# Performance work log

Hardware: AMD Instinct MI355X
Metric: run time of the kernel (lower is better)

Reference implementation:

```python
import jax, jax.numpy as jnp
import numpy as np


def setup_inputs() -> dict:
    key = jax.random.key(0)
    ks = jax.random.split(key, 4)
    B, C, D, H, W = 2, 128, 16, 16, 16
    scale = 1.0 / np.sqrt(C)
    x = jax.random.normal(ks[0], (B, C, D, H, W), dtype=jnp.float32)
    Wq = jax.random.normal(ks[1], (C, C), dtype=jnp.float32) * scale
    Wk = jax.random.normal(ks[2], (C, C), dtype=jnp.float32) * scale
    Wv = jax.random.normal(ks[3], (C, C), dtype=jnp.float32) * scale
    bq = jnp.zeros((C,), jnp.float32)
    bk = jnp.zeros((C,), jnp.float32)
    bv = jnp.zeros((C,), jnp.float32)
    gamma = jnp.asarray(0.3, jnp.float32)
    return {"x": x, "Wq": Wq, "bq": bq, "Wk": Wk, "bk": bk, "Wv": Wv, "bv": bv, "gamma": gamma}


def reference(x, Wq, bq, Wk, bk, Wv, bv, gamma):
    B, C, D, H, W = x.shape
    N = D * H * W
    xf = x.reshape(B, C, N)  # flatten spatial dims
    # 1x1x1 Conv3d == per-voxel channel mixing
    q = jnp.einsum('oc,bcn->bon', Wq, xf) + bq[:, None]
    k = jnp.einsum('oc,bcn->bon', Wk, xf) + bk[:, None]
    v = jnp.einsum('oc,bcn->bon', Wv, xf) + bv[:, None]
    # attn[b,n,m] = sum_c q[b,c,n] * k[b,c,m], custom 1.3 scale, softmax over m
    attn = jax.nn.softmax(jnp.einsum('bcn,bcm->bnm', q, k) * 1.3, axis=2)
    # out = v @ attn^T : out[b,c,n] = sum_m v[b,c,m] * attn[b,n,m]
    out = jnp.einsum('bcm,bnm->bcn', v, attn)
    return x + gamma * out.reshape(B, C, D, H, W)
```

## Files before the change

### kernel.cpp

```cpp
#include <hip/hip_runtime.h>
#include <hip/hip_bf16.h>

typedef __bf16 bf16x8 __attribute__((ext_vector_type(8)));
typedef __bf16 bf16x4 __attribute__((ext_vector_type(4)));
typedef float  floatx4 __attribute__((ext_vector_type(4)));


#define QSCALE 1.8755035f

__global__ __launch_bounds__(128) void proj_kernel(
    const float* __restrict__ x,
    const float* __restrict__ Wq, const float* __restrict__ bq,
    const float* __restrict__ Wk, const float* __restrict__ bk,
    const float* __restrict__ Wv, const float* __restrict__ bv,
    __bf16* __restrict__ qT, __bf16* __restrict__ kT, __bf16* __restrict__ vT2)
{
    constexpr int C = 128, N = 4096;
    const int b = blockIdx.z, which = blockIdx.y, n0 = blockIdx.x * 32;
    const int tid = threadIdx.x;
    const int wv = tid >> 6, lane = tid & 63, l15 = lane & 15, quad = lane >> 4;
    const float* W    = (which == 0) ? Wq : (which == 1) ? Wk : Wv;
    const float* bias = (which == 0) ? bq : (which == 1) ? bk : bv;

    __shared__ __bf16 xhi[32][136];
    __shared__ __bf16 xlo[32][136];
    __shared__ __bf16 v_lds[128][40];

    #pragma unroll
    for (int rep = 0; rep < 8; ++rep) {
        const int j = tid + rep * 128;
        const int c = j >> 3, nl4 = (j & 7) * 4;
        const float4 xv = *(const float4*)(x + (size_t)(b * C + c) * N + n0 + nl4);
        #pragma unroll
        for (int r = 0; r < 4; ++r) {
            const float v = (&xv.x)[r];
            const __bf16 h = (__bf16)v;
            xhi[nl4 + r][c] = h;
            xlo[nl4 + r][c] = (__bf16)(v - (float)h);
        }
    }
    __syncthreads();

    bf16x8 xbh[4], xbl[4];
    #pragma unroll
    for (int kk = 0; kk < 4; ++kk) {
        xbh[kk] = *(bf16x8*)(&xhi[wv * 16 + l15][kk * 32 + quad * 8]);
        xbl[kk] = *(bf16x8*)(&xlo[wv * 16 + l15][kk * 32 + quad * 8]);
    }

    floatx4 acc[8];
    const floatx4 fz = {0.f, 0.f, 0.f, 0.f};
    #pragma unroll
    for (int t = 0; t < 8; ++t) acc[t] = fz;

    #pragma unroll
    for (int kk = 0; kk < 4; ++kk)
        #pragma unroll
        for (int ct = 0; ct < 8; ++ct) {
            const float* wp = W + (size_t)(ct * 16 + l15) * C + kk * 32 + quad * 8;
            const float4 w0 = *(const float4*)wp;
            const float4 w1 = *(const float4*)(wp + 4);
            bf16x8 ahi, alo;
            #pragma unroll
            for (int r = 0; r < 4; ++r) {
                const float v0 = (&w0.x)[r]; const __bf16 h0 = (__bf16)v0;
                ahi[r] = h0; alo[r] = (__bf16)(v0 - (float)h0);
                const float v1 = (&w1.x)[r]; const __bf16 h1 = (__bf16)v1;
                ahi[4 + r] = h1; alo[4 + r] = (__bf16)(v1 - (float)h1);
            }
            acc[ct] = __builtin_amdgcn_mfma_f32_16x16x32_bf16(ahi, xbh[kk], acc[ct], 0, 0, 0);
            acc[ct] = __builtin_amdgcn_mfma_f32_16x16x32_bf16(alo, xbh[kk], acc[ct], 0, 0, 0);
            acc[ct] = __builtin_amdgcn_mfma_f32_16x16x32_bf16(ahi, xbl[kk], acc[ct], 0, 0, 0);
        }

    const int n = n0 + wv * 16 + l15;
    if (which < 2) {
        __bf16* dst = (which == 0) ? qT : kT;
        #pragma unroll
        for (int ct = 0; ct < 8; ++ct) {
            const float4 b4 = *(const float4*)(bias + ct * 16 + quad * 4);
            bf16x4 o;
            #pragma unroll
            for (int r = 0; r < 4; ++r) o[r] = (__bf16)(acc[ct][r] + (&b4.x)[r]);
            *(bf16x4*)(dst + (size_t)(b * N + n) * C + ct * 16 + quad * 4) = o;
        }
    } else {
        #pragma unroll
        for (int ct = 0; ct < 8; ++ct) {
            const float4 b4 = *(const float4*)(bias + ct * 16 + quad * 4);
            #pragma unroll
            for (int r = 0; r < 4; ++r)
                v_lds[ct * 16 + quad * 4 + r][wv * 16 + l15] = (__bf16)(acc[ct][r] + (&b4.x)[r]);
        }
        __syncthreads();
        #pragma unroll
        for (int rep = 0; rep < 4; ++rep) {
            const int j = tid + rep * 128;
            const int c = j >> 2, m8 = (j & 3) * 8;
            *(bf16x8*)(vT2 + (size_t)(b * C + c) * N + n0 + m8) = *(bf16x8*)(&v_lds[c][m8]);
        }
    }
}

template <int NSPLIT, bool PARTIAL>
__global__ __launch_bounds__(256, 2) void flash_kernel(
    const __bf16* __restrict__ qT, const __bf16* __restrict__ kT,
    const __bf16* __restrict__ vT2, const float* __restrict__ x,
    const float* __restrict__ gamma_p, __bf16* __restrict__ Opart,
    float* __restrict__ ml, float* __restrict__ out)
{
    constexpr int C = 128, N = 4096, Bn = 2;
    const int bid = blockIdx.x;
    const int r7 = bid & 7;
    const int b = r7 >> 2;
    const int rest = (bid >> 3) * 4 + (r7 & 3);
    const int nt = rest & 63, split = rest >> 6;
    const int n0 = nt * 64;
    const int tid = threadIdx.x;
    const int wv = tid >> 6, lane = tid & 63, l15 = lane & 15, quad = lane >> 4;

    __shared__ __bf16 k_s[64][136];
    __shared__ __bf16 v_s[128][72];
    __shared__ __bf16 p_s[4][16][72];

    const int n = n0 + wv * 16 + l15;
    bf16x8 qb[4];
    #pragma unroll
    for (int kk = 0; kk < 4; ++kk)
        qb[kk] = *(const bf16x8*)(qT + (size_t)(b * N + n) * C + kk * 32 + quad * 8);

    float m_i = -3.0e38f, l_i = 0.f;
    floatx4 Oacc[8];
    const floatx4 fz = {0.f, 0.f, 0.f, 0.f};
    #pragma unroll
    for (int t = 0; t < 8; ++t) Oacc[t] = fz;

    const __bf16* kB = kT  + (size_t)b * N * C;
    const __bf16* vB = vT2 + (size_t)b * C * N;
    constexpr int ITERS = (N / NSPLIT) / 64;
    const int mbeg = split * (N / NSPLIT);

    bf16x8 kpre[4], vpre[4];
    #pragma unroll
    for (int rep = 0; rep < 4; ++rep) {
        const int kj = tid + rep * 256;
        kpre[rep] = *(const bf16x8*)(kB + (size_t)(mbeg + (kj >> 4)) * C + (kj & 15) * 8);
        const int vj = tid + rep * 256;
        vpre[rep] = *(const bf16x8*)(vB + (size_t)(vj >> 3) * N + mbeg + (vj & 7) * 8);
    }

    for (int it = 0; it < ITERS; ++it) {
        __syncthreads();
        #pragma unroll
        for (int rep = 0; rep < 4; ++rep) {
            const int kj = tid + rep * 256;
            *(bf16x8*)(&k_s[kj >> 4][(kj & 15) * 8]) = kpre[rep];
            const int vj = tid + rep * 256;
            *(bf16x8*)(&v_s[vj >> 3][(vj & 7) * 8]) = vpre[rep];
        }
        __syncthreads();

        if (it + 1 < ITERS) {
            const int m1 = mbeg + (it + 1) * 64;
            #pragma unroll
            for (int rep = 0; rep < 4; ++rep) {
                const int kj = tid + rep * 256;
                kpre[rep] = *(const bf16x8*)(kB + (size_t)(m1 + (kj >> 4)) * C + (kj & 15) * 8);
                const int vj = tid + rep * 256;
                vpre[rep] = *(const bf16x8*)(vB + (size_t)(vj >> 3) * N + m1 + (vj & 7) * 8);
            }
        }

        floatx4 S[4];
        #pragma unroll
        for (int ct = 0; ct < 4; ++ct) S[ct] = fz;
        #pragma unroll
        for (int kk = 0; kk < 4; ++kk)
            #pragma unroll
            for (int ct = 0; ct < 4; ++ct) {
                const bf16x8 a = *(bf16x8*)(&k_s[ct * 16 + l15][kk * 32 + quad * 8]);
                S[ct] = __builtin_amdgcn_mfma_f32_16x16x32_bf16(a, qb[kk], S[ct], 0, 0, 0);
            }

        float rmax = -3.0e38f;
        #pragma unroll
        for (int ct = 0; ct < 4; ++ct)
            #pragma unroll
            for (int r = 0; r < 4; ++r) {
                const float v = S[ct][r] * QSCALE;
                S[ct][r] = v;
                rmax = fmaxf(rmax, v);
            }
        rmax = fmaxf(rmax, __shfl_xor(rmax, 16, 64));
        rmax = fmaxf(rmax, __shfl_xor(rmax, 32, 64));

        const float mn = fmaxf(m_i, rmax);
        const float alpha = exp2f(m_i - mn);
        m_i = mn;

        float rsum = 0.f;
        #pragma unroll
        for (int ct = 0; ct < 4; ++ct)
            #pragma unroll
            for (int r = 0; r < 4; ++r) {
                const float p = exp2f(S[ct][r] - m_i);
                S[ct][r] = p;
                rsum += p;
            }
        rsum += __shfl_xor(rsum, 16, 64);
        rsum += __shfl_xor(rsum, 32, 64);
        l_i = l_i * alpha + rsum;

        #pragma unroll
        for (int t = 0; t < 8; ++t)
            #pragma unroll
            for (int r = 0; r < 4; ++r) Oacc[t][r] *= alpha;

        #pragma unroll
        for (int ct = 0; ct < 4; ++ct) {
            bf16x4 pk;
            #pragma unroll
            for (int r = 0; r < 4; ++r) pk[r] = (__bf16)S[ct][r];
            *(bf16x4*)(&p_s[wv][l15][ct * 16 + quad * 4]) = pk;
        }

        #pragma unroll
        for (int kk = 0; kk < 2; ++kk) {
            const bf16x8 pb = *(bf16x8*)(&p_s[wv][l15][kk * 32 + quad * 8]);
            #pragma unroll
            for (int ct = 0; ct < 8; ++ct) {
                const bf16x8 a = *(bf16x8*)(&v_s[ct * 16 + l15][kk * 32 + quad * 8]);
                Oacc[ct] = __builtin_amdgcn_mfma_f32_16x16x32_bf16(a, pb, Oacc[ct], 0, 0, 0);
            }
        }
    }

    if (PARTIAL) {
        __bf16* Op = Opart + (((size_t)split * Bn + b) * N + n) * C;
        #pragma unroll
        for (int ct = 0; ct < 8; ++ct) {
            bf16x4 o;
            #pragma unroll
            for (int r = 0; r < 4; ++r) o[r] = (__bf16)Oacc[ct][r];
            *(bf16x4*)(Op + ct * 16 + quad * 4) = o;
        }
        if (quad == 0) {
            float* mlp = ml + (((size_t)split * Bn + b) * N + n) * 2;
            mlp[0] = m_i; mlp[1] = l_i;
        }
    } else {
        const float sc = 1.f / l_i;
        const float gamma = gamma_p[0];
        #pragma unroll
        for (int ct = 0; ct < 8; ++ct)
            #pragma unroll
            for (int r = 0; r < 4; ++r) {
                const int c = ct * 16 + quad * 4 + r;
                const size_t idx = ((size_t)b * C + c) * N + n;
                out[idx] = x[idx] + gamma * Oacc[ct][r] * sc;
            }
    }
}

__global__ __launch_bounds__(256) void combine_kernel(
    const __bf16* __restrict__ Opart, const float* __restrict__ ml,
    const float* __restrict__ x, const float* __restrict__ gamma_p,
    float* __restrict__ out)
{
    constexpr int C = 128, N = 4096, Bn = 2, S = 4;
    const int b = blockIdx.y, n0 = blockIdx.x * 32;
    const int tid = threadIdx.x;
    __shared__ float cf[S][32];
    __shared__ float ot[32][132];

    if (tid < 32) {
        const int n = n0 + tid;
        float ms[S], ls[S];
        #pragma unroll
        for (int s = 0; s < S; ++s) {
            const float* mlp = ml + (((size_t)s * Bn + b) * N + n) * 2;
            ms[s] = mlp[0]; ls[s] = mlp[1];
        }
        float M = -3.0e38f;
        #pragma unroll
        for (int s = 0; s < S; ++s) M = fmaxf(M, ms[s]);
        float L = 0.f, e[S];
        #pragma unroll
        for (int s = 0; s < S; ++s) { e[s] = exp2f(ms[s] - M); L += e[s] * ls[s]; }
        const float inv = 1.f / L;
        #pragma unroll
        for (int s = 0; s < S; ++s) cf[s][tid] = e[s] * inv;
    }
    __syncthreads();

    #pragma unroll
    for (int rep = 0; rep < 2; ++rep) {
        const int j = tid + rep * 256;
        const int nl = j >> 4, c8 = (j & 15) * 8;
        float acc[8] = {0, 0, 0, 0, 0, 0, 0, 0};
        #pragma unroll
        for (int s = 0; s < S; ++s) {
            const float c0 = cf[s][nl];
            const bf16x8 ov = *(const bf16x8*)(Opart + (((size_t)s * Bn + b) * N + n0 + nl) * C + c8);
            #pragma unroll
            for (int t = 0; t < 8; ++t) acc[t] += c0 * (float)ov[t];
        }
        *(float4*)(&ot[nl][c8])     = *(float4*)(&acc[0]);
        *(float4*)(&ot[nl][c8 + 4]) = *(float4*)(&acc[4]);
    }
    __syncthreads();

    const int nl = tid & 31, cbase = tid >> 5;
    const float gamma = gamma_p[0];
    #pragma unroll
    for (int k = 0; k < 16; ++k) {
        const int c = cbase * 16 + k;
        const size_t idx = ((size_t)b * C + c) * N + n0 + nl;
        out[idx] = x[idx] + gamma * ot[nl][c];
    }
}

extern "C" void kernel_launch(void* const* d_in, const int* in_sizes, int n_in,
                              void* d_out, int out_size, void* d_ws, size_t ws_size,
                              hipStream_t stream) {
    const float* x     = (const float*)d_in[0];
    const float* Wq    = (const float*)d_in[1];
    const float* bq    = (const float*)d_in[2];
    const float* Wk    = (const float*)d_in[3];
    const float* bk    = (const float*)d_in[4];
    const float* Wv    = (const float*)d_in[5];
    const float* bv    = (const float*)d_in[6];
    const float* gamma = (const float*)d_in[7];
    float* out = (float*)d_out;

    constexpr int Bn = 2, C = 128, N = 4096;
    constexpr size_t QKV = (size_t)Bn * N * C;
    __bf16* qT    = (__bf16*)d_ws;
    __bf16* kT    = qT + QKV;
    __bf16* vT2   = kT + QKV;
    __bf16* Opart = vT2 + QKV;
    float*  ml    = (float*)(Opart + (size_t)4 * Bn * N * C);
    const size_t need = (char*)(ml + (size_t)4 * Bn * N * 2) - (char*)d_ws;

    proj_kernel<<<dim3(N / 32, 3, Bn), 128, 0, stream>>>(
        x, Wq, bq, Wk, bk, Wv, bv, qT, kT, vT2);

    if (ws_size >= need) {
        flash_kernel<4, true><<<64 * 4 * Bn, 256, 0, stream>>>(
            qT, kT, vT2, x, gamma, Opart, ml, out);
        combine_kernel<<<dim3(N / 32, Bn), 256, 0, stream>>>(
            Opart, ml, x, gamma, out);
    } else {
        flash_kernel<1, false><<<64 * 1 * Bn, 256, 0, stream>>>(
            qT, kT, vT2, x, gamma, nullptr, nullptr, out);
    }
}
```

Before: 128.2 us.

## Process two query tiles per wave and raise KV split count to eight

Each wave now handles 32 query rows (two 16-row tiles) instead of 16, so every K and V fragment read from LDS feeds two MFMAs. This doubles reuse of shared-memory loads and halves K/V global traffic per query. To keep the grid large enough, the KV dimension is split into 8 parts instead of 4, with a templated combine kernel. The cost is higher register pressure from doubled accumulators, plus more partial output written and merged by the combine step.

New measurement: 125.7 us. No clear change (-1.9%).

```diff
diff --git a/kernel.cpp b/kernel.cpp
--- a/kernel.cpp
+++ b/kernel.cpp
@@ -114,26 +114,28 @@
     const int r7 = bid & 7;
     const int b = r7 >> 2;
     const int rest = (bid >> 3) * 4 + (r7 & 3);
-    const int nt = rest & 63, split = rest >> 6;
-    const int n0 = nt * 64;
+    const int nt = rest / NSPLIT, split = rest % NSPLIT;
+    const int n0 = nt * 128;
     const int tid = threadIdx.x;
     const int wv = tid >> 6, lane = tid & 63, l15 = lane & 15, quad = lane >> 4;
 
     __shared__ __bf16 k_s[64][136];
     __shared__ __bf16 v_s[128][72];
-    __shared__ __bf16 p_s[4][16][72];
-
-    const int n = n0 + wv * 16 + l15;
-    bf16x8 qb[4];
-    #pragma unroll
-    for (int kk = 0; kk < 4; ++kk)
-        qb[kk] = *(const bf16x8*)(qT + (size_t)(b * N + n) * C + kk * 32 + quad * 8);
-
-    float m_i = -3.0e38f, l_i = 0.f;
-    floatx4 Oacc[8];
+    __shared__ __bf16 p_s[4][32][72];
+
+    const int nA = n0 + wv * 32 + l15;
+    bf16x8 qbA[4], qbB[4];
+    #pragma unroll
+    for (int kk = 0; kk < 4; ++kk) {
+        qbA[kk] = *(const bf16x8*)(qT + (size_t)(b * N + nA) * C + kk * 32 + quad * 8);
+        qbB[kk] = *(const bf16x8*)(qT + (size_t)(b * N + nA + 16) * C + kk * 32 + quad * 8);
+    }
+
+    float mA = -3.0e38f, lA = 0.f, mB = -3.0e38f, lB = 0.f;
+    floatx4 OA[8], OB[8];
     const floatx4 fz = {0.f, 0.f, 0.f, 0.f};
     #pragma unroll
-    for (int t = 0; t < 8; ++t) Oacc[t] = fz;
+    for (int t = 0; t < 8; ++t) { OA[t] = fz; OB[t] = fz; }
 
     const __bf16* kB = kT  + (size_t)b * N * C;
     const __bf16* vB = vT2 + (size_t)b * C * N;
@@ -171,103 +173,118 @@
             }
         }
 
-        floatx4 S[4];
-        #pragma unroll
-        for (int ct = 0; ct < 4; ++ct) S[ct] = fz;
+        floatx4 SA[4], SB[4];
+        #pragma unroll
+        for (int ct = 0; ct < 4; ++ct) { SA[ct] = fz; SB[ct] = fz; }
         #pragma unroll
         for (int kk = 0; kk < 4; ++kk)
             #pragma unroll
             for (int ct = 0; ct < 4; ++ct) {
                 const bf16x8 a = *(bf16x8*)(&k_s[ct * 16 + l15][kk * 32 + quad * 8]);
-                S[ct] = __builtin_amdgcn_mfma_f32_16x16x32_bf16(a, qb[kk], S[ct], 0, 0, 0);
-            }
-
-        float rmax = -3.0e38f;
+                SA[ct] = __builtin_amdgcn_mfma_f32_16x16x32_bf16(a, qbA[kk], SA[ct], 0, 0, 0);
+                SB[ct] = __builtin_amdgcn_mfma_f32_16x16x32_bf16(a, qbB[kk], SB[ct], 0, 0, 0);
+            }
+
+        float rmaxA = -3.0e38f, rmaxB = -3.0e38f;
         #pragma unroll
         for (int ct = 0; ct < 4; ++ct)
             #pragma unroll
             for (int r = 0; r < 4; ++r) {
-                const float v = S[ct][r] * QSCALE;
-                S[ct][r] = v;
-                rmax = fmaxf(rmax, v);
-            }
-        rmax = fmaxf(rmax, __shfl_xor(rmax, 16, 64));
-        rmax = fmaxf(rmax, __shfl_xor(rmax, 32, 64));
-
-        const float mn = fmaxf(m_i, rmax);
-        const float alpha = exp2f(m_i - mn);
-        m_i = mn;
-
-        float rsum = 0.f;
+                const float vA = SA[ct][r] * QSCALE; SA[ct][r] = vA; rmaxA = fmaxf(rmaxA, vA);
+                const float vB2 = SB[ct][r] * QSCALE; SB[ct][r] = vB2; rmaxB = fmaxf(rmaxB, vB2);
+            }
+        rmaxA = fmaxf(rmaxA, __shfl_xor(rmaxA, 16, 64));
+        rmaxA = fmaxf(rmaxA, __shfl_xor(rmaxA, 32, 64));
+        rmaxB = fmaxf(rmaxB, __shfl_xor(rmaxB, 16, 64));
+        rmaxB = fmaxf(rmaxB, __shfl_xor(rmaxB, 32, 64));
+
+        const float mnA = fmaxf(mA, rmaxA);
+        const float alphaA = exp2f(mA - mnA);
+        mA = mnA;
+        const float mnB = fmaxf(mB, rmaxB);
+        const float alphaB = exp2f(mB - mnB);
+        mB = mnB;
+
+        float rsumA = 0.f, rsumB = 0.f;
         #pragma unroll
         for (int ct = 0; ct < 4; ++ct)
             #pragma unroll
             for (int r = 0; r < 4; ++r) {
-                const float p = exp2f(S[ct][r] - m_i);
-                S[ct][r] = p;
-                rsum += p;
-            }
-        rsum += __shfl_xor(rsum, 16, 64);
-        rsum += __shfl_xor(rsum, 32, 64);
-        l_i = l_i * alpha + rsum;
+                const float pA = exp2f(SA[ct][r] - mA); SA[ct][r] = pA; rsumA += pA;
+                const float pB = exp2f(SB[ct][r] - mB); SB[ct][r] = pB; rsumB += pB;
+            }
+        rsumA += __shfl_xor(rsumA, 16, 64);
+        rsumA += __shfl_xor(rsumA, 32, 64);
+        rsumB += __shfl_xor(rsumB, 16, 64);
+        rsumB += __shfl_xor(rsumB, 32, 64);
+        lA = lA * alphaA + rsumA;
+        lB = lB * alphaB + rsumB;
 
         #pragma unroll
         for (int t = 0; t < 8; ++t)
             #pragma unroll
-            for (int r = 0; r < 4; ++r) Oacc[t][r] *= alpha;
+            for (int r = 0; r < 4; ++r) { OA[t][r] *= alphaA; OB[t][r] *= alphaB; }
 
         #pragma unroll
         for (int ct = 0; ct < 4; ++ct) {
-            bf16x4 pk;
-            #pragma unroll
-            for (int r = 0; r < 4; ++r) pk[r] = (__bf16)S[ct][r];
-            *(bf16x4*)(&p_s[wv][l15][ct * 16 + quad * 4]) = pk;
+            bf16x4 pkA, pkB;
+            #pragma unroll
+            for (int r = 0; r < 4; ++r) { pkA[r] = (__bf16)SA[ct][r]; pkB[r] = (__bf16)SB[ct][r]; }
+            *(bf16x4*)(&p_s[wv][l15][ct * 16 + quad * 4])      = pkA;
+            *(bf16x4*)(&p_s[wv][16 + l15][ct * 16 + quad * 4]) = pkB;
         }
 
         #pragma unroll
         for (int kk = 0; kk < 2; ++kk) {
-            const bf16x8 pb = *(bf16x8*)(&p_s[wv][l15][kk * 32 + quad * 8]);
+            const bf16x8 pbA = *(bf16x8*)(&p_s[wv][l15][kk * 32 + quad * 8]);
+            const bf16x8 pbB = *(bf16x8*)(&p_s[wv][16 + l15][kk * 32 + quad * 8]);
             #pragma unroll
             for (int ct = 0; ct < 8; ++ct) {
                 const bf16x8 a = *(bf16x8*)(&v_s[ct * 16 + l15][kk * 32 + quad * 8]);
-                Oacc[ct] = __builtin_amdgcn_mfma_f32_16x16x32_bf16(a, pb, Oacc[ct], 0, 0, 0);
+                OA[ct] = __builtin_amdgcn_mfma_f32_16x16x32_bf16(a, pbA, OA[ct], 0, 0, 0);
+                OB[ct] = __builtin_amdgcn_mfma_f32_16x16x32_bf16(a, pbB, OB[ct], 0, 0, 0);
             }
         }
     }
 
     if (PARTIAL) {
-        __bf16* Op = Opart + (((size_t)split * Bn + b) * N + n) * C;
+        __bf16* OpA = Opart + (((size_t)split * Bn + b) * N + nA) * C;
+        __bf16* OpB = OpA + (size_t)16 * C;
         #pragma unroll
         for (int ct = 0; ct < 8; ++ct) {
-            bf16x4 o;
-            #pragma unroll
-            for (int r = 0; r < 4; ++r) o[r] = (__bf16)Oacc[ct][r];
-            *(bf16x4*)(Op + ct * 16 + quad * 4) = o;
+            bf16x4 oA, oB;
+            #pragma unroll
+            for (int r = 0; r < 4; ++r) { oA[r] = (__bf16)OA[ct][r]; oB[r] = (__bf16)OB[ct][r]; }
+            *(bf16x4*)(OpA + ct * 16 + quad * 4) = oA;
+            *(bf16x4*)(OpB + ct * 16 + quad * 4) = oB;
         }
         if (quad == 0) {
-            float* mlp = ml + (((size_t)split * Bn + b) * N + n) * 2;
-            mlp[0] = m_i; mlp[1] = l_i;
+            float* mlp = ml + (((size_t)split * Bn + b) * N + nA) * 2;
+            mlp[0] = mA; mlp[1] = lA;
+            mlp[32] = mB; mlp[33] = lB;
         }
     } else {
-        const float sc = 1.f / l_i;
+        const float scA = 1.f / lA, scB = 1.f / lB;
         const float gamma = gamma_p[0];
         #pragma unroll
         for (int ct = 0; ct < 8; ++ct)
             #pragma unroll
             for (int r = 0; r < 4; ++r) {
                 const int c = ct * 16 + quad * 4 + r;
-                const size_t idx = ((size_t)b * C + c) * N + n;
-                out[idx] = x[idx] + gamma * Oacc[ct][r] * sc;
+                const size_t iA = ((size_t)b * C + c) * N + nA;
+                out[iA]      = x[iA]      + gamma * OA[ct][r] * scA;
+                out[iA + 16] = x[iA + 16] + gamma * OB[ct][r] * scB;
             }
     }
 }
 
+template <int S>
 __global__ __launch_bounds__(256) void combine_kernel(
     const __bf16* __restrict__ Opart, const float* __restrict__ ml,
     const float* __restrict__ x, const float* __restrict__ gamma_p,
     float* __restrict__ out)
 {
-    constexpr int C = 128, N = 4096, Bn = 2, S = 4;
+    constexpr int C = 128, N = 4096, Bn = 2;
     const int b = blockIdx.y, n0 = blockIdx.x * 32;
     const int tid = threadIdx.x;
     __shared__ float cf[S][32];
@@ -339,19 +356,26 @@
     __bf16* kT    = qT + QKV;
     __bf16* vT2   = kT + QKV;
     __bf16* Opart = vT2 + QKV;
-    float*  ml    = (float*)(Opart + (size_t)4 * Bn * N * C);
-    const size_t need = (char*)(ml + (size_t)4 * Bn * N * 2) - (char*)d_ws;
+    float* ml8 = (float*)(Opart + (size_t)8 * Bn * N * C);
+    float* ml4 = (float*)(Opart + (size_t)4 * Bn * N * C);
+    const size_t need8 = (char*)(ml8 + (size_t)8 * Bn * N * 2) - (char*)d_ws;
+    const size_t need4 = (char*)(ml4 + (size_t)4 * Bn * N * 2) - (char*)d_ws;
 
     proj_kernel<<<dim3(N / 32, 3, Bn), 128, 0, stream>>>(
         x, Wq, bq, Wk, bk, Wv, bv, qT, kT, vT2);
 
-    if (ws_size >= need) {
-        flash_kernel<4, true><<<64 * 4 * Bn, 256, 0, stream>>>(
-            qT, kT, vT2, x, gamma, Opart, ml, out);
-        combine_kernel<<<dim3(N / 32, Bn), 256, 0, stream>>>(
-            Opart, ml, x, gamma, out);
+    if (ws_size >= need8) {
+        flash_kernel<8, true><<<32 * 8 * Bn, 256, 0, stream>>>(
+            qT, kT, vT2, x, gamma, Opart, ml8, out);
+        combine_kernel<8><<<dim3(N / 32, Bn), 256, 0, stream>>>(
+            Opart, ml8, x, gamma, out);
+    } else if (ws_size >= need4) {
+        flash_kernel<4, true><<<32 * 4 * Bn, 256, 0, stream>>>(
+            qT, kT, vT2, x, gamma, Opart, ml4, out);
+        combine_kernel<4><<<dim3(N / 32, Bn), 256, 0, stream>>>(
+            Opart, ml4, x, gamma, out);
     } else {
-        flash_kernel<1, false><<<64 * 1 * Bn, 256, 0, stream>>>(
+        flash_kernel<1, false><<<32 * 1 * Bn, 256, 0, stream>>>(
             qT, kT, vT2, x, gamma, nullptr, nullptr, out);
     }
 }
```
